# Optimization experiments

Measured on AMD Instinct MI355X. Metric: run time of the kernel, lower is better.

Reference implementation:

```python
import jax, jax.numpy as jnp
import numpy as np
from jax import lax

B, S, H, E, TOP_K = 4, 2048, 8192, 256, 8

def setup_inputs() -> dict:
    key = jax.random.key(0)
    kx, kw = jax.random.split(key)
    x = jax.random.normal(kx, (B, S, H), dtype=jnp.float32)
    # Dense kernel init scale ~ 1/sqrt(H)
    W_router = jax.random.normal(kw, (H, E), dtype=jnp.float32) * (1.0 / np.sqrt(H))
    return {"x": x, "W_router": W_router}

def reference(x, W_router):
    # router_logits: [B, S, E]
    router_logits = jnp.einsum('bsh,he->bse', x, W_router)
    top_logits, top_indices = lax.top_k(router_logits, k=TOP_K)  # [B,S,K]
    routing_weights = jax.nn.softmax(top_logits, axis=-1)        # [B,S,K]
    return routing_weights, top_indices, router_logits
```

## Files before the change

### kernel.cpp

```cpp
#include <hip/hip_runtime.h>
#include <math.h>
#include <float.h>

typedef _Float16 half8 __attribute__((ext_vector_type(8)));
typedef float f32x4 __attribute__((ext_vector_type(4)));

namespace {
constexpr int kH = 8192, kE = 256, kTopK = 8, kTok = 8192;
constexpr int kIdxOff = kTok * kTopK;
constexpr int kLogitsOff = 2 * kTok * kTopK;
constexpr int kBM = 128, kBN = 128, kBK = 32;
constexpr int kPadH = 40;
constexpr int kCand = 16;
constexpr float kEps = 5e-5f;
constexpr float kInvScale = 1.0f / 262144.0f;
constexpr size_t kWtF   = (size_t)kE * kH;
constexpr size_t kWtlF  = kWtF + (size_t)kE * kH / 2;
constexpr size_t kPartF = kWtF + (size_t)kE * kH;
constexpr size_t kPartStride = (size_t)kTok * kE;
}

__device__ __forceinline__ void gld16(const _Float16* g, _Float16* l) {
    __builtin_amdgcn_global_load_lds(
        (const __attribute__((address_space(1))) void*)g,
        (__attribute__((address_space(3))) void*)l, 16, 0, 0);
}

__device__ __forceinline__ int kswz(int e, int k) {
    return (k & ~31) | (((((k >> 3) & 3) ^ ((e >> 1) & 3))) << 3) | (k & 7);
}

__global__ __launch_bounds__(1024)
void prep_w(const float* __restrict__ W, float* __restrict__ Wt,
            _Float16* __restrict__ Wth, _Float16* __restrict__ Wtl) {
    __shared__ float tile[32][33];
    const int k0 = blockIdx.x * 32, e0 = blockIdx.y * 32;
    const int tx = threadIdx.x, ty = threadIdx.y;
    tile[ty][tx] = W[(size_t)(k0 + ty) * kE + (e0 + tx)];
    __syncthreads();
    const float v = tile[tx][ty];
    const int e = e0 + ty, k = k0 + tx;
    Wt[(size_t)e * kH + k] = v;
    const float vs = v * 256.0f;
    const _Float16 h = (_Float16)vs;
    const size_t os = (size_t)e * kH + kswz(e, k);
    Wth[os] = h;
    Wtl[os] = (_Float16)(vs - (float)h);
}

__global__ __launch_bounds__(256, 2)
void router_gemm_mfma(const float* __restrict__ x,
                      const _Float16* __restrict__ Wth,
                      const _Float16* __restrict__ Wtl,
                      float* __restrict__ p0, float* __restrict__ pws,
                      int kchunk)
{
    __shared__ __align__(16) _Float16 sxh[kBM * kPadH];
    __shared__ __align__(16) _Float16 sxl[kBM * kPadH];
    __shared__ __align__(16) _Float16 swh[kBN * kBK];
    __shared__ __align__(16) _Float16 swl[kBN * kBK];

    const int tid  = threadIdx.x;
    const int lane = tid & 63;
    const int w    = tid >> 6;
    const int wm   = w >> 1, wn = w & 1;
    const int t0   = blockIdx.x * kBM;
    const int e0   = blockIdx.y * kBN;
    const int kbase = blockIdx.z * kchunk;
    const int nsteps = kchunk / kBK;

    f32x4 acc[4][4];
    #pragma unroll
    for (int m = 0; m < 4; ++m)
        #pragma unroll
        for (int n = 0; n < 4; ++n) {
            acc[m][n][0] = 0.f; acc[m][n][1] = 0.f;
            acc[m][n][2] = 0.f; acc[m][n][3] = 0.f;
        }

    const size_t wro0 = (size_t)(e0 + (w << 4) + (lane >> 2)) * kH
                        + kbase + ((lane & 3) << 3);
    const size_t wro1 = wro0 + (size_t)64 * kH;
    _Float16* lwh0 = swh + (w << 9);
    _Float16* lwh1 = swh + (w << 9) + 2048;
    _Float16* lwl0 = swl + (w << 9);
    _Float16* lwl1 = swl + (w << 9) + 2048;

    const int srow = tid >> 1;
    const int scg  = (tid & 1) << 4;
    const float* xp = x + (size_t)(t0 + srow) * kH + kbase + scg;

    float4 xv0 = *reinterpret_cast<const float4*>(xp);
    float4 xv1 = *reinterpret_cast<const float4*>(xp + 4);
    float4 xv2 = *reinterpret_cast<const float4*>(xp + 8);
    float4 xv3 = *reinterpret_cast<const float4*>(xp + 12);

    const int fr  = lane & 15;
    const int q   = lane >> 4;
    const int fkA = q << 3;
    const int fkB = ((q ^ ((fr >> 1) & 3)) << 3);

    for (int t = 0; t < nsteps; ++t) {
        const size_t ko = (size_t)t << 5;
        gld16(Wth + wro0 + ko, lwh0);
        gld16(Wth + wro1 + ko, lwh1);
        gld16(Wtl + wro0 + ko, lwl0);
        gld16(Wtl + wro1 + ko, lwl1);

        float xf[16];
        xf[0]=xv0.x; xf[1]=xv0.y; xf[2]=xv0.z; xf[3]=xv0.w;
        xf[4]=xv1.x; xf[5]=xv1.y; xf[6]=xv1.z; xf[7]=xv1.w;
        xf[8]=xv2.x; xf[9]=xv2.y; xf[10]=xv2.z; xf[11]=xv2.w;
        xf[12]=xv3.x; xf[13]=xv3.y; xf[14]=xv3.z; xf[15]=xv3.w;
        half8 h0, h1, l0, l1;
        #pragma unroll
        for (int i = 0; i < 8; ++i) {
            const float sA = xf[i] * 1024.0f;
            const _Float16 hA = (_Float16)sA;
            h0[i] = hA; l0[i] = (_Float16)(sA - (float)hA);
            const float sB = xf[i + 8] * 1024.0f;
            const _Float16 hB = (_Float16)sB;
            h1[i] = hB; l1[i] = (_Float16)(sB - (float)hB);
        }
        *reinterpret_cast<half8*>(&sxh[srow * kPadH + scg])     = h0;
        *reinterpret_cast<half8*>(&sxh[srow * kPadH + scg + 8]) = h1;
        *reinterpret_cast<half8*>(&sxl[srow * kPadH + scg])     = l0;
        *reinterpret_cast<half8*>(&sxl[srow * kPadH + scg + 8]) = l1;

        __syncthreads();

        if (t + 1 < nsteps) {
            const float* nx = xp + ((size_t)(t + 1) << 5);
            xv0 = *reinterpret_cast<const float4*>(nx);
            xv1 = *reinterpret_cast<const float4*>(nx + 4);
            xv2 = *reinterpret_cast<const float4*>(nx + 8);
            xv3 = *reinterpret_cast<const float4*>(nx + 12);
        }

        half8 ah[4], al[4];
        #pragma unroll
        for (int m = 0; m < 4; ++m) {
            const int arow = (wm << 6) + (m << 4) + fr;
            ah[m] = *reinterpret_cast<const half8*>(&sxh[arow * kPadH + fkA]);
            al[m] = *reinterpret_cast<const half8*>(&sxl[arow * kPadH + fkA]);
        }
        #pragma unroll
        for (int n = 0; n < 4; ++n) {
            const int brow = (wn << 6) + (n << 4) + fr;
            const half8 bh = *reinterpret_cast<const half8*>(&swh[brow * kBK + fkB]);
            const half8 bl = *reinterpret_cast<const half8*>(&swl[brow * kBK + fkB]);
            #pragma unroll
            for (int m = 0; m < 4; ++m) {
                acc[m][n] = __builtin_amdgcn_mfma_f32_16x16x32_f16(ah[m], bh, acc[m][n], 0, 0, 0);
                acc[m][n] = __builtin_amdgcn_mfma_f32_16x16x32_f16(ah[m], bl, acc[m][n], 0, 0, 0);
                acc[m][n] = __builtin_amdgcn_mfma_f32_16x16x32_f16(al[m], bh, acc[m][n], 0, 0, 0);
            }
        }
        __syncthreads();
    }

    float* dst = (blockIdx.z == 0) ? p0 : (pws + (size_t)(blockIdx.z - 1) * kPartStride);
    const int r0 = (lane >> 4) << 2;
    const int c0 = lane & 15;
    #pragma unroll
    for (int m = 0; m < 4; ++m)
        #pragma unroll
        for (int n = 0; n < 4; ++n) {
            const int col = e0 + (wn << 6) + (n << 4) + c0;
            #pragma unroll
            for (int r = 0; r < 4; ++r) {
                const int row = t0 + (wm << 6) + (m << 4) + r0 + r;
                dst[(size_t)row * kE + col] = acc[m][n][r] * kInvScale;
            }
        }
}

#define ARGMAX_ROUND(r)                                                        \
    {                                                                          \
        float bv = v0; int bi = (lane << 2);                                   \
        if (v1 > bv) { bv = v1; bi = (lane << 2) + 1; }                        \
        if (v2 > bv) { bv = v2; bi = (lane << 2) + 2; }                        \
        if (v3 > bv) { bv = v3; bi = (lane << 2) + 3; }                        \
        _Pragma("unroll")                                                      \
        for (int off = 32; off > 0; off >>= 1) {                               \
            const float ov = __shfl_xor(bv, off, 64);                          \
            const int   oi = __shfl_xor(bi, off, 64);                          \
            if (ov > bv || (ov == bv && oi < bi)) { bv = ov; bi = oi; }        \
        }                                                                      \
        if (lane == (r)) { myv = bv; myi = bi; }                               \
        if ((bi >> 2) == lane) {                                               \
            const int m = bi & 3;                                              \
            if      (m == 0) v0 = -FLT_MAX;                                    \
            else if (m == 1) v1 = -FLT_MAX;                                    \
            else if (m == 2) v2 = -FLT_MAX;                                    \
            else             v3 = -FLT_MAX;                                    \
        }                                                                      \
    }

__global__ __launch_bounds__(256)
void combine_select(const float* __restrict__ x, const float* __restrict__ Wt,
                    const float* __restrict__ pws, float* __restrict__ out,
                    int npart)
{
    const int lane = threadIdx.x & 63;
    const int w    = threadIdx.x >> 6;
    const int row  = blockIdx.x * 4 + w;
    float* logits = out + kLogitsOff;
    const size_t rb = (size_t)row * kE + (lane << 2);

    float4 s = *reinterpret_cast<const float4*>(logits + rb);
    for (int p = 0; p < npart; ++p) {
        const float4 q = *reinterpret_cast<const float4*>(pws + (size_t)p * kPartStride + rb);
        s.x += q.x; s.y += q.y; s.z += q.z; s.w += q.w;
    }
    *reinterpret_cast<float4*>(logits + rb) = s;

    float v0 = s.x, v1 = s.y, v2 = s.z, v3 = s.w;
    float myv = -FLT_MAX; int myi = -1;

    #pragma unroll
    for (int r = 0; r < 9; ++r) ARGMAX_ROUND(r)

    const float nv = __shfl_down(myv, 1, 64);
    const unsigned long long amb = __ballot(lane < 8 && (myv - nv) < kEps);

    if (amb == 0ull) {
        const float m = __shfl(myv, 0, 64);
        const float e = (lane < kTopK) ? expf(myv - m) : 0.f;
        float t = e;
        #pragma unroll
        for (int off = 1; off < 8; off <<= 1) t += __shfl_xor(t, off, 64);
        if (lane < kTopK) {
            out[(size_t)row * kTopK + lane]           = e / t;
            out[kIdxOff + (size_t)row * kTopK + lane] = (float)myi;
        }
    } else {
        #pragma unroll
        for (int r = 9; r < kCand; ++r) ARGMAX_ROUND(r)

        const float* xr = x + (size_t)row * kH;
        double dv = -1.0e300;
        #pragma unroll 1
        for (int cg = 0; cg < kCand; cg += 4) {
            const int i0 = __shfl(myi, cg + 0, 64);
            const int i1 = __shfl(myi, cg + 1, 64);
            const int i2 = __shfl(myi, cg + 2, 64);
            const int i3 = __shfl(myi, cg + 3, 64);
            const float* w0 = Wt + (size_t)i0 * kH;
            const float* w1 = Wt + (size_t)i1 * kH;
            const float* w2 = Wt + (size_t)i2 * kH;
            const float* w3 = Wt + (size_t)i3 * kH;
            double a0 = 0.0, a1 = 0.0, a2 = 0.0, a3 = 0.0;
            for (int k = (lane << 2); k < kH; k += 256) {
                const float4 xv = *reinterpret_cast<const float4*>(xr + k);
                const float4 q0 = *reinterpret_cast<const float4*>(w0 + k);
                const float4 q1 = *reinterpret_cast<const float4*>(w1 + k);
                const float4 q2 = *reinterpret_cast<const float4*>(w2 + k);
                const float4 q3 = *reinterpret_cast<const float4*>(w3 + k);
                a0 = fma((double)xv.x, (double)q0.x, a0);
                a1 = fma((double)xv.x, (double)q1.x, a1);
                a2 = fma((double)xv.x, (double)q2.x, a2);
                a3 = fma((double)xv.x, (double)q3.x, a3);
                a0 = fma((double)xv.y, (double)q0.y, a0);
                a1 = fma((double)xv.y, (double)q1.y, a1);
                a2 = fma((double)xv.y, (double)q2.y, a2);
                a3 = fma((double)xv.y, (double)q3.y, a3);
                a0 = fma((double)xv.z, (double)q0.z, a0);
                a1 = fma((double)xv.z, (double)q1.z, a1);
                a2 = fma((double)xv.z, (double)q2.z, a2);
                a3 = fma((double)xv.z, (double)q3.z, a3);
                a0 = fma((double)xv.w, (double)q0.w, a0);
                a1 = fma((double)xv.w, (double)q1.w, a1);
                a2 = fma((double)xv.w, (double)q2.w, a2);
                a3 = fma((double)xv.w, (double)q3.w, a3);
            }
            #pragma unroll
            for (int off = 32; off > 0; off >>= 1) {
                a0 += __shfl_xor(a0, off, 64);
                a1 += __shfl_xor(a1, off, 64);
                a2 += __shfl_xor(a2, off, 64);
                a3 += __shfl_xor(a3, off, 64);
            }
            if (lane == cg + 0) dv = a0;
            if (lane == cg + 1) dv = a1;
            if (lane == cg + 2) dv = a2;
            if (lane == cg + 3) dv = a3;
        }

        double cv = dv; int ci = myi;
        double mx = 0.0, ssum = 0.0, keepv = 0.0; int keepi = 0;
        #pragma unroll 1
        for (int r = 0; r < kTopK; ++r) {
            double bv = cv; int bi = ci;
            #pragma unroll
            for (int off = 32; off > 0; off >>= 1) {
                const double ov = __shfl_xor(bv, off, 64);
                const int    oi = __shfl_xor(bi, off, 64);
                if (ov > bv || (ov == bv && oi < bi)) { bv = ov; bi = oi; }
            }
            if (r == 0) mx = bv;
            ssum += exp(bv - mx);
            if (lane == r) { keepv = bv; keepi = bi; }
            if (ci == bi) cv = -1.0e300;
        }
        if (lane < kTopK) {
            out[(size_t)row * kTopK + lane]           = (float)(exp(keepv - mx) / ssum);
            out[kIdxOff + (size_t)row * kTopK + lane] = (float)keepi;
        }
    }
}

extern "C" void kernel_launch(void* const* d_in, const int* in_sizes, int n_in,
                              void* d_out, int out_size, void* d_ws, size_t ws_size,
                              hipStream_t stream) {
    const float* x  = (const float*)d_in[0];
    const float* Wr = (const float*)d_in[1];
    float* out = (float*)d_out;
    float* Wt  = (float*)d_ws;
    _Float16* Wth = (_Float16*)((float*)d_ws + kWtF);
    _Float16* Wtl = (_Float16*)((float*)d_ws + kWtlF);
    float* pws = (float*)d_ws + kPartF;
    (void)in_sizes; (void)n_in; (void)out_size;

    const size_t need8 = (kPartF + 7 * kPartStride) * sizeof(float);
    const int nkc = (ws_size >= need8) ? 8 : 4;
    const int kchunk = kH / nkc;

    hipLaunchKernelGGL(prep_w, dim3(kH / 32, kE / 32), dim3(32, 32), 0, stream,
                       Wr, Wt, Wth, Wtl);
    hipLaunchKernelGGL(router_gemm_mfma, dim3(kTok / kBM, kE / kBN, nkc), dim3(256),
                       0, stream, x, Wth, Wtl, out + kLogitsOff, pws, kchunk);
    hipLaunchKernelGGL(combine_select, dim3(kTok / 4), dim3(256), 0, stream,
                       x, Wt, pws, out, nkc - 1);
}
```

Before: 247.6 us.

## Double-buffer LDS tiles in router GEMM, drop W swizzle, halve split-K

Switches the router GEMM's shared-memory staging to two buffers, so the next K-step's W tiles and converted x tiles are written while MFMAs run on the current step. This removes one barrier per iteration and hides load latency. The XOR swizzle on the W layout is removed, so B-fragment reads use a plain offset, which may bring LDS bank conflicts back. The split-K factor drops from 8 to 4 (or 2), cutting partial-sum traffic in the combine step but giving fewer blocks; doubled LDS may also lower occupancy.

Measured after the change: 230.3 us. 1.08x faster.

```diff
diff --git a/kernel.cpp b/kernel.cpp
--- a/kernel.cpp
+++ b/kernel.cpp
@@ -26,10 +26,6 @@
         (__attribute__((address_space(3))) void*)l, 16, 0, 0);
 }
 
-__device__ __forceinline__ int kswz(int e, int k) {
-    return (k & ~31) | (((((k >> 3) & 3) ^ ((e >> 1) & 3))) << 3) | (k & 7);
-}
-
 __global__ __launch_bounds__(1024)
 void prep_w(const float* __restrict__ W, float* __restrict__ Wt,
             _Float16* __restrict__ Wth, _Float16* __restrict__ Wtl) {
@@ -39,13 +35,12 @@
     tile[ty][tx] = W[(size_t)(k0 + ty) * kE + (e0 + tx)];
     __syncthreads();
     const float v = tile[tx][ty];
-    const int e = e0 + ty, k = k0 + tx;
-    Wt[(size_t)e * kH + k] = v;
+    const size_t o = (size_t)(e0 + ty) * kH + (k0 + tx);
+    Wt[o] = v;
     const float vs = v * 256.0f;
     const _Float16 h = (_Float16)vs;
-    const size_t os = (size_t)e * kH + kswz(e, k);
-    Wth[os] = h;
-    Wtl[os] = (_Float16)(vs - (float)h);
+    Wth[o] = h;
+    Wtl[o] = (_Float16)(vs - (float)h);
 }
 
 __global__ __launch_bounds__(256, 2)
@@ -55,10 +50,10 @@
                       float* __restrict__ p0, float* __restrict__ pws,
                       int kchunk)
 {
-    __shared__ __align__(16) _Float16 sxh[kBM * kPadH];
-    __shared__ __align__(16) _Float16 sxl[kBM * kPadH];
-    __shared__ __align__(16) _Float16 swh[kBN * kBK];
-    __shared__ __align__(16) _Float16 swl[kBN * kBK];
+    __shared__ __align__(16) _Float16 sxh[2][kBM * kPadH];
+    __shared__ __align__(16) _Float16 sxl[2][kBM * kPadH];
+    __shared__ __align__(16) _Float16 swh[2][kBN * kBK];
+    __shared__ __align__(16) _Float16 swl[2][kBN * kBK];
 
     const int tid  = threadIdx.x;
     const int lane = tid & 63;
@@ -81,74 +76,89 @@
     const size_t wro0 = (size_t)(e0 + (w << 4) + (lane >> 2)) * kH
                         + kbase + ((lane & 3) << 3);
     const size_t wro1 = wro0 + (size_t)64 * kH;
-    _Float16* lwh0 = swh + (w << 9);
-    _Float16* lwh1 = swh + (w << 9) + 2048;
-    _Float16* lwl0 = swl + (w << 9);
-    _Float16* lwl1 = swl + (w << 9) + 2048;
+    const int wl0 = (w << 9);
+    const int wl1 = (w << 9) + 2048;
 
     const int srow = tid >> 1;
     const int scg  = (tid & 1) << 4;
     const float* xp = x + (size_t)(t0 + srow) * kH + kbase + scg;
 
-    float4 xv0 = *reinterpret_cast<const float4*>(xp);
-    float4 xv1 = *reinterpret_cast<const float4*>(xp + 4);
-    float4 xv2 = *reinterpret_cast<const float4*>(xp + 8);
-    float4 xv3 = *reinterpret_cast<const float4*>(xp + 12);
-
-    const int fr  = lane & 15;
-    const int q   = lane >> 4;
-    const int fkA = q << 3;
-    const int fkB = ((q ^ ((fr >> 1) & 3)) << 3);
+    float4 xr0, xr1, xr2, xr3;
+
+#define CVT_STORE(B)                                                           \
+    {                                                                          \
+        float xf[16];                                                          \
+        xf[0]=xr0.x; xf[1]=xr0.y; xf[2]=xr0.z; xf[3]=xr0.w;                    \
+        xf[4]=xr1.x; xf[5]=xr1.y; xf[6]=xr1.z; xf[7]=xr1.w;                    \
+        xf[8]=xr2.x; xf[9]=xr2.y; xf[10]=xr2.z; xf[11]=xr2.w;                  \
+        xf[12]=xr3.x; xf[13]=xr3.y; xf[14]=xr3.z; xf[15]=xr3.w;                \
+        half8 h0, h1, l0, l1;                                                  \
+        _Pragma("unroll")                                                      \
+        for (int i = 0; i < 8; ++i) {                                          \
+            const float sA = xf[i] * 1024.0f;                                  \
+            const _Float16 hA = (_Float16)sA;                                  \
+            h0[i] = hA; l0[i] = (_Float16)(sA - (float)hA);                    \
+            const float sB = xf[i + 8] * 1024.0f;                              \
+            const _Float16 hB = (_Float16)sB;                                  \
+            h1[i] = hB; l1[i] = (_Float16)(sB - (float)hB);                    \
+        }                                                                      \
+        *reinterpret_cast<half8*>(&sxh[B][srow * kPadH + scg])     = h0;       \
+        *reinterpret_cast<half8*>(&sxh[B][srow * kPadH + scg + 8]) = h1;       \
+        *reinterpret_cast<half8*>(&sxl[B][srow * kPadH + scg])     = l0;       \
+        *reinterpret_cast<half8*>(&sxl[B][srow * kPadH + scg + 8]) = l1;       \
+    }
+
+    gld16(Wth + wro0, &swh[0][wl0]);
+    gld16(Wth + wro1, &swh[0][wl1]);
+    gld16(Wtl + wro0, &swl[0][wl0]);
+    gld16(Wtl + wro1, &swl[0][wl1]);
+    xr0 = *reinterpret_cast<const float4*>(xp);
+    xr1 = *reinterpret_cast<const float4*>(xp + 4);
+    xr2 = *reinterpret_cast<const float4*>(xp + 8);
+    xr3 = *reinterpret_cast<const float4*>(xp + 12);
+    CVT_STORE(0)
+    if (nsteps > 1) {
+        xr0 = *reinterpret_cast<const float4*>(xp + 32);
+        xr1 = *reinterpret_cast<const float4*>(xp + 36);
+        xr2 = *reinterpret_cast<const float4*>(xp + 40);
+        xr3 = *reinterpret_cast<const float4*>(xp + 44);
+    }
+    __syncthreads();
+
+    const int fr = lane & 15;
+    const int fk = (lane >> 4) << 3;
 
     for (int t = 0; t < nsteps; ++t) {
-        const size_t ko = (size_t)t << 5;
-        gld16(Wth + wro0 + ko, lwh0);
-        gld16(Wth + wro1 + ko, lwh1);
-        gld16(Wtl + wro0 + ko, lwl0);
-        gld16(Wtl + wro1 + ko, lwl1);
-
-        float xf[16];
-        xf[0]=xv0.x; xf[1]=xv0.y; xf[2]=xv0.z; xf[3]=xv0.w;
-        xf[4]=xv1.x; xf[5]=xv1.y; xf[6]=xv1.z; xf[7]=xv1.w;
-        xf[8]=xv2.x; xf[9]=xv2.y; xf[10]=xv2.z; xf[11]=xv2.w;
-        xf[12]=xv3.x; xf[13]=xv3.y; xf[14]=xv3.z; xf[15]=xv3.w;
-        half8 h0, h1, l0, l1;
-        #pragma unroll
-        for (int i = 0; i < 8; ++i) {
-            const float sA = xf[i] * 1024.0f;
-            const _Float16 hA = (_Float16)sA;
-            h0[i] = hA; l0[i] = (_Float16)(sA - (float)hA);
-            const float sB = xf[i + 8] * 1024.0f;
-            const _Float16 hB = (_Float16)sB;
-            h1[i] = hB; l1[i] = (_Float16)(sB - (float)hB);
-        }
-        *reinterpret_cast<half8*>(&sxh[srow * kPadH + scg])     = h0;
-        *reinterpret_cast<half8*>(&sxh[srow * kPadH + scg + 8]) = h1;
-        *reinterpret_cast<half8*>(&sxl[srow * kPadH + scg])     = l0;
-        *reinterpret_cast<half8*>(&sxl[srow * kPadH + scg + 8]) = l1;
-
-        __syncthreads();
+        const int cur = t & 1, nxt = cur ^ 1;
 
         if (t + 1 < nsteps) {
-            const float* nx = xp + ((size_t)(t + 1) << 5);
-            xv0 = *reinterpret_cast<const float4*>(nx);
-            xv1 = *reinterpret_cast<const float4*>(nx + 4);
-            xv2 = *reinterpret_cast<const float4*>(nx + 8);
-            xv3 = *reinterpret_cast<const float4*>(nx + 12);
+            const size_t ko = (size_t)(t + 1) << 5;
+            gld16(Wth + wro0 + ko, &swh[nxt][wl0]);
+            gld16(Wth + wro1 + ko, &swh[nxt][wl1]);
+            gld16(Wtl + wro0 + ko, &swl[nxt][wl0]);
+            gld16(Wtl + wro1 + ko, &swl[nxt][wl1]);
+            CVT_STORE(nxt)
+            if (t + 2 < nsteps) {
+                const float* nx = xp + ((size_t)(t + 2) << 5);
+                xr0 = *reinterpret_cast<const float4*>(nx);
+                xr1 = *reinterpret_cast<const float4*>(nx + 4);
+                xr2 = *reinterpret_cast<const float4*>(nx + 8);
+                xr3 = *reinterpret_cast<const float4*>(nx + 12);
+            }
         }
 
         half8 ah[4], al[4];
         #pragma unroll
         for (int m = 0; m < 4; ++m) {
             const int arow = (wm << 6) + (m << 4) + fr;
-            ah[m] = *reinterpret_cast<const half8*>(&sxh[arow * kPadH + fkA]);
-            al[m] = *reinterpret_cast<const half8*>(&sxl[arow * kPadH + fkA]);
+            ah[m] = *reinterpret_cast<const half8*>(&sxh[cur][arow * kPadH + fk]);
+            al[m] = *reinterpret_cast<const half8*>(&sxl[cur][arow * kPadH + fk]);
         }
         #pragma unroll
         for (int n = 0; n < 4; ++n) {
             const int brow = (wn << 6) + (n << 4) + fr;
-            const half8 bh = *reinterpret_cast<const half8*>(&swh[brow * kBK + fkB]);
-            const half8 bl = *reinterpret_cast<const half8*>(&swl[brow * kBK + fkB]);
+            const half8 bh = *reinterpret_cast<const half8*>(&swh[cur][brow * kBK + fk]);
+            const half8 bl = *reinterpret_cast<const half8*>(&swl[cur][brow * kBK + fk]);
             #pragma unroll
             for (int m = 0; m < 4; ++m) {
                 acc[m][n] = __builtin_amdgcn_mfma_f32_16x16x32_f16(ah[m], bh, acc[m][n], 0, 0, 0);
@@ -156,8 +166,10 @@
                 acc[m][n] = __builtin_amdgcn_mfma_f32_16x16x32_f16(al[m], bh, acc[m][n], 0, 0, 0);
             }
         }
+
         __syncthreads();
     }
+#undef CVT_STORE
 
     float* dst = (blockIdx.z == 0) ? p0 : (pws + (size_t)(blockIdx.z - 1) * kPartStride);
     const int r0 = (lane >> 4) << 2;
@@ -322,8 +334,8 @@
     float* pws = (float*)d_ws + kPartF;
     (void)in_sizes; (void)n_in; (void)out_size;
 
-    const size_t need8 = (kPartF + 7 * kPartStride) * sizeof(float);
-    const int nkc = (ws_size >= need8) ? 8 : 4;
+    const size_t need4 = (kPartF + 3 * kPartStride) * sizeof(float);
+    const int nkc = (ws_size >= need4) ? 4 : 2;
     const int kchunk = kH / nkc;
 
     hipLaunchKernelGGL(prep_w, dim3(kH / 32, kE / 32), dim3(32, 32), 0, stream,
```
